# Kernel tuning notes

Measured on AMD Instinct MI355X. Metric: run time of the kernel, lower is better.

## Reference

```python
import jax, jax.numpy as jnp
import numpy as np

W = 192      # image width (seq len for attn1)
HN = 192     # H * N (seq len for attn2)
C = 128      # hidden_dim
NHEAD = 8


def setup_inputs() -> dict:
    key = jax.random.key(0)
    ks = jax.random.split(key, 12)
    sc = 0.05  # small init so softmax is well-conditioned
    feat = jax.random.normal(ks[0], (W, 2 * HN, C), jnp.float32)
    pos = jax.random.normal(ks[1], (2 * W - 1, C), jnp.float32)
    pos_y = jax.random.normal(ks[2], (2 * HN - 1, C), jnp.float32)
    i = jnp.arange(W)
    pos_indexes = (i[:, None] - i[None, :] + W - 1).reshape(-1).astype(jnp.int32)
    j = jnp.arange(HN)
    pos_indexes_y = (j[:, None] - j[None, :] + HN - 1).reshape(-1).astype(jnp.int32)
    return {
        "feat": feat,
        "pos": pos,
        "pos_y": pos_y,
        "ln_w": jnp.ones((C,), jnp.float32),
        "ln_b": jnp.zeros((C,), jnp.float32),
        "w_in1": jax.random.normal(ks[3], (3 * C, C), jnp.float32) * sc,
        "b_in1": jnp.zeros((3 * C,), jnp.float32),
        "w_out1": jax.random.normal(ks[4], (C, C), jnp.float32) * sc,
        "b_out1": jnp.zeros((C,), jnp.float32),
        "w_in2": jax.random.normal(ks[5], (3 * C, C), jnp.float32) * sc,
        "b_in2": jnp.zeros((3 * C,), jnp.float32),
        "w_out2": jax.random.normal(ks[6], (C, C), jnp.float32) * sc,
        "b_out2": jnp.zeros((C,), jnp.float32),
        "pos_indexes": pos_indexes,
        "pos_indexes_y": pos_indexes_y,
    }


def _layernorm(x, g, b, eps=1e-5):
    m = x.mean(-1, keepdims=True)
    v = ((x - m) ** 2).mean(-1, keepdims=True)
    return (x - m) / jnp.sqrt(v + eps) * g + b


def _rel_attn(x, pos_enc, pos_idx, w_in, b_in, w_out, b_out):
    # x: [w, bsz, c]; pos_enc: [2w-1, c]; pos_idx: [w*w]
    w, bsz, c = x.shape
    hd = c // NHEAD
    scale = float(hd) ** -0.5
    q, k, v = jnp.split(x @ w_in.T + b_in, 3, axis=-1)
    pe = pos_enc[pos_idx].reshape(w, w, c)           # [w, w, c] relative pos
    q_r, k_r = jnp.split(pe @ w_in[: 2 * c].T + b_in[: 2 * c], 2, axis=-1)
    q = (q * scale).reshape(w, bsz, NHEAD, hd)
    k = k.reshape(w, bsz, NHEAD, hd)
    v = v.reshape(w, bsz, NHEAD, hd)
    q_r = (q_r * scale).reshape(w, w, NHEAD, hd)
    k_r = k_r.reshape(w, w, NHEAD, hd)
    # content-content + content-pos + pos-content -> [bsz, nhead, w, w]
    attn = (jnp.einsum('wnec,vnec->newv', q, k)
            + jnp.einsum('wnec,wvec->newv', q, k_r)
            + jnp.einsum('vnec,wvec->newv', k, q_r))
    attn = jax.nn.softmax(attn, axis=-1)
    out = jnp.einsum('newv,vnec->wnec', attn, v).reshape(w, bsz, c)
    return out @ w_out.T + b_out


def reference(feat, pos, pos_y, ln_w, ln_b,
              w_in1, b_in1, w_out1, b_out1,
              w_in2, b_in2, w_out2, b_out2,
              pos_indexes, pos_indexes_y):
    w, h2, c = feat.shape
    f2 = _layernorm(feat, ln_w, ln_b)
    # [W, 2HN, C] -> [HN, 2W, C]: attention along vertical (H) axis
    f2 = f2.reshape(w, 2, h2 // 2, c).transpose(2, 1, 0, 3).reshape(h2 // 2, 2 * w, c)
    f2 = _rel_attn(f2, pos_y, pos_indexes_y, w_in2, b_in2, w_out2, b_out2)
    # back to [W, 2HN, C]: attention along horizontal (W) axis
    f2 = f2.reshape(h2 // 2, 2, w, c).transpose(2, 1, 0, 3).reshape(w, h2, c)
    f2 = _rel_attn(f2, pos, pos_indexes, w_in1, b_in1, w_out1, b_out1)
    return feat + f2
```

## Files before the change

kernel.cpp:

```cpp
#include <hip/hip_runtime.h>
#include <hip/hip_bf16.h>


typedef unsigned short u16;
typedef short bf16x8 __attribute__((ext_vector_type(8)));
typedef float f32x4 __attribute__((ext_vector_type(4)));
typedef float f32x16 __attribute__((ext_vector_type(16)));

__device__ inline u16 f2bf(float f) {
    union { float f; unsigned u; } a; a.f = f;
    unsigned u = a.u;
    unsigned r = u + 0x7FFFu + ((u >> 16) & 1u);
    return (u16)(r >> 16);
}
__device__ inline float bf2f(u16 x) {
    union { unsigned u; float f; } a; a.u = ((unsigned)x) << 16;
    return a.f;
}

__global__ __launch_bounds__(256) void ln_kernel(const float* __restrict__ feat,
                                                 const float* __restrict__ g,
                                                 const float* __restrict__ bta,
                                                 u16* __restrict__ x2) {
    int wid = threadIdx.x >> 6, lane = threadIdx.x & 63;
    int r = blockIdx.x * 4 + wid;
    const float* row = feat + (size_t)r * 128;
    float v0 = row[lane], v1 = row[lane + 64];
    float s = v0 + v1;
    for (int m = 1; m < 64; m <<= 1) s += __shfl_xor(s, m);
    float mean = s * (1.0f / 128.0f);
    float d0 = v0 - mean, d1 = v1 - mean;
    float vs = d0 * d0 + d1 * d1;
    for (int m = 1; m < 64; m <<= 1) vs += __shfl_xor(vs, m);
    float rstd = rsqrtf(vs * (1.0f / 128.0f) + 1e-5f);
    int w = r / 384, rem = r % 384;
    int out_r = (rem % 192) * 384 + (rem / 192) * 192 + w;
    u16* orow = x2 + (size_t)out_r * 128;
    orow[lane]      = f2bf(d0 * rstd * g[lane] + bta[lane]);
    orow[lane + 64] = f2bf(d1 * rstd * g[lane + 64] + bta[lane + 64]);
}

__global__ __launch_bounds__(256) void posproj_kernel(const float* __restrict__ pos,
                                                      const float* __restrict__ w_in,
                                                      const float* __restrict__ b_in,
                                                      u16* __restrict__ qr,
                                                      u16* __restrict__ kr) {
    int d = blockIdx.x, t = threadIdx.x;
    if (d == 383) {
        if (t < 128)      { int e = t >> 4,  j = t & 15;  qr[(e * 384 + 383) * 16 + j] = 0; }
        else              { int t2 = t - 128; int e = t2 >> 4, j = t2 & 15; kr[(e * 384 + 383) * 16 + j] = 0; }
        return;
    }
    __shared__ float prow[128];
    if (t < 128) prow[t] = pos[d * 128 + t];
    __syncthreads();
    const float* wrow = w_in + t * 128;
    float acc = b_in[t];
    #pragma unroll 8
    for (int k = 0; k < 128; ++k) acc += prow[k] * wrow[k];
    int which = t >> 7, e = (t >> 4) & 7, j = t & 15;
    if (which == 0) qr[(e * 384 + d) * 16 + j] = f2bf(acc * 0.25f);
    else            kr[(e * 384 + d) * 16 + j] = f2bf(acc);
}

__global__ __launch_bounds__(256) void qkv_gemm(const u16* __restrict__ X,
                                                const float* __restrict__ Wn,
                                                const float* __restrict__ bias,
                                                u16* __restrict__ Qo,
                                                u16* __restrict__ Ko,
                                                u16* __restrict__ Vo) {
    __shared__ u16 a_lds[128][136];
    __shared__ u16 w_lds[64][136];
    int tid = threadIdx.x;
    int m0 = blockIdx.y * 128, n0 = blockIdx.x * 64;
    #pragma unroll
    for (int i = 0; i < 8; ++i) {
        int idx = tid + 256 * i;
        int row = idx >> 4, c8 = (idx & 15) * 8;
        *(int4*)&a_lds[row][c8] = *(const int4*)&X[(size_t)(m0 + row) * 128 + c8];
    }
    #pragma unroll
    for (int i = 0; i < 8; ++i) {
        int idx = tid + 256 * i;
        int row = idx >> 5, c4 = (idx & 31) * 4;
        float4 f = *(const float4*)&Wn[(size_t)(n0 + row) * 128 + c4];
        uint2 p;
        p.x = (unsigned)f2bf(f.x) | ((unsigned)f2bf(f.y) << 16);
        p.y = (unsigned)f2bf(f.z) | ((unsigned)f2bf(f.w) << 16);
        *(uint2*)&w_lds[row][c4] = p;
    }
    __syncthreads();
    int lane = tid & 63, wid = tid >> 6;
    int wr = (wid >> 1) * 64, wc = (wid & 1) * 32;
    int kg = lane >> 4, l15 = lane & 15;
    f32x4 acc[4][2];
    #pragma unroll
    for (int i = 0; i < 4; ++i)
        #pragma unroll
        for (int j = 0; j < 2; ++j) acc[i][j] = (f32x4){0.f, 0.f, 0.f, 0.f};
    #pragma unroll
    for (int kk = 0; kk < 4; ++kk) {
        int kof = kk * 32 + kg * 8;
        bf16x8 a[4], b[2];
        #pragma unroll
        for (int i = 0; i < 4; ++i) a[i] = *(const bf16x8*)&a_lds[wr + i * 16 + l15][kof];
        #pragma unroll
        for (int j = 0; j < 2; ++j) b[j] = *(const bf16x8*)&w_lds[wc + j * 16 + l15][kof];
        #pragma unroll
        for (int i = 0; i < 4; ++i)
            #pragma unroll
            for (int j = 0; j < 2; ++j)
                acc[i][j] = __builtin_amdgcn_mfma_f32_16x16x32_bf16(a[i], b[j], acc[i][j], 0, 0, 0);
    }
    #pragma unroll
    for (int i = 0; i < 4; ++i)
        #pragma unroll
        for (int j = 0; j < 2; ++j) {
            int col_g = n0 + wc + j * 16 + l15;
            float bv = bias[col_g];
            int which = col_g >> 7, e = (col_g >> 4) & 7, d = col_g & 15;
            u16* dst = which == 0 ? Qo : (which == 1 ? Ko : Vo);
            float scl = which == 0 ? 0.25f : 1.0f;
            #pragma unroll
            for (int ii = 0; ii < 4; ++ii) {
                int row_g = m0 + wr + i * 16 + kg * 4 + ii;
                int batch = row_g % 384, sq = row_g / 384;
                dst[((size_t)(batch * 8 + e) * 192 + sq) * 16 + d] = f2bf((acc[i][j][ii] + bv) * scl);
            }
        }
}

__global__ __launch_bounds__(512, 6) void attn_kernel(const u16* __restrict__ Qg,
                                                      const u16* __restrict__ Kg,
                                                      const u16* __restrict__ Vg,
                                                      const u16* __restrict__ qr_g,
                                                      const u16* __restrict__ kr_g,
                                                      u16* __restrict__ Og) {
    __shared__ u16 sc[96][200];
    __shared__ u16 Qs[96][16];
    __shared__ u16 Ks[192][16];
    __shared__ u16 Vt[16][200];
    int tid = threadIdx.x, lane = tid & 63, wid = tid >> 6;
    int half = blockIdx.x, e = blockIdx.y, b = blockIdx.z;
    int w0 = half * 96;
    size_t base = ((size_t)b * 8 + e) * 192 * 16;

    if (tid < 192) { int row = tid >> 1, h8 = (tid & 1) * 8;
        *(int4*)&Qs[row][h8] = *(const int4*)&Qg[base + (size_t)(w0 + row) * 16 + h8]; }
    if (tid >= 128) { int t2 = tid - 128; int row = t2 >> 1, h8 = (t2 & 1) * 8;
        *(int4*)&Ks[row][h8] = *(const int4*)&Kg[base + (size_t)row * 16 + h8]; }
    #pragma unroll
    for (int i = 0; i < 6; ++i) { int idx = tid + 512 * i;
        Vt[idx & 15][idx >> 4] = Vg[base + idx]; }
    __syncthreads();

    int lo = lane & 31, hi = lane >> 5, hi8 = hi * 8;

    #pragma unroll
    for (int it = 0; it < 3; ++it) {
        int t = wid + 8 * it;
        if (t < 18) {
            int wt = t / 6, vt = t % 6;
            bf16x8 a  = *(const bf16x8*)&Qs[wt * 32 + lo][hi8];
            bf16x8 bb = *(const bf16x8*)&Ks[vt * 32 + lo][hi8];
            f32x16 acc = {};
            acc = __builtin_amdgcn_mfma_f32_32x32x16_bf16(a, bb, acc, 0, 0, 0);
            #pragma unroll
            for (int ii = 0; ii < 16; ++ii) {
                int row = wt * 32 + (ii & 3) + 8 * (ii >> 2) + 4 * hi;
                sc[row][vt * 32 + lo] = f2bf(acc[ii]);
            }
        }
    }
    __syncthreads();

    #pragma unroll
    for (int it = 0; it < 3; ++it) {
        int t = wid + 8 * it;
        if (t < 21) {
            int wt = t / 7, dj = t % 7;
            int d0 = w0 + wt * 32 + dj * 32;
            bf16x8 a  = *(const bf16x8*)&Qs[wt * 32 + lo][hi8];
            bf16x8 bb = *(const bf16x8*)(kr_g + ((size_t)e * 384 + d0 + lo) * 16 + hi8);
            f32x16 acc = {};
            acc = __builtin_amdgcn_mfma_f32_32x32x16_bf16(a, bb, acc, 0, 0, 0);
            int off = 4 * hi - lo + (wt * 32 + 191 - (dj * 32) - wt * 32);
            int vbase = w0 + wt * 32 + 191 - d0 - lo + 4 * hi;
            int wlb = wt * 32 + 4 * hi;
            (void)off;
            #pragma unroll
            for (int ii = 0; ii < 16; ++ii) {
                int rr = (ii & 3) + 8 * (ii >> 2);
                int v = vbase + rr;
                if ((unsigned)v < 192u) {
                    u16* p = &sc[wlb + rr][v];
                    *p = f2bf(bf2f(*p) + acc[ii]);
                }
            }
        }
    }
    __syncthreads();

    #pragma unroll
    for (int it = 0; it < 3; ++it) {
        int t = wid + 8 * it;
        if (t < 24) {
            int vt = t >> 2, dj = t & 3;
            int V0 = vt * 32;
            int d0 = w0 + 160 - V0 + dj * 32;
            bf16x8 a  = *(const bf16x8*)(qr_g + ((size_t)e * 384 + d0 + lo) * 16 + hi8);
            bf16x8 bb = *(const bf16x8*)&Ks[V0 + lo][hi8];
            f32x16 acc = {};
            acc = __builtin_amdgcn_mfma_f32_32x32x16_bf16(a, bb, acc, 0, 0, 0);
            int v = V0 + lo;
            int wlb = d0 + 4 * hi + v - 191 - w0;
            #pragma unroll
            for (int ii = 0; ii < 16; ++ii) {
                int rr = (ii & 3) + 8 * (ii >> 2);
                int wl = wlb + rr;
                if ((unsigned)wl < 96u) {
                    u16* p = &sc[wl][v];
                    *p = f2bf(bf2f(*p) + acc[ii]);
                }
            }
        }
    }
    __syncthreads();

    #pragma unroll
    for (int p = 0; p < 3; ++p) {
        int r = wid * 12 + p * 4 + (lane >> 4);
        int j = lane & 15;
        u16* rowp = &sc[r][j * 12];
        float sum = 0.f;
        #pragma unroll
        for (int k = 0; k < 12; ++k) {
            float ev = __expf(bf2f(rowp[k]));
            sum += ev;
            rowp[k] = f2bf(ev);
        }
        sum += __shfl_xor(sum, 1);
        sum += __shfl_xor(sum, 2);
        sum += __shfl_xor(sum, 4);
        sum += __shfl_xor(sum, 8);
        if (j == 0) *(float*)&sc[r][196] = 1.0f / sum;
    }
    __syncthreads();

    if (wid < 6) {
        int l15 = lane & 15, kg = lane >> 4;
        f32x4 acc = (f32x4){0.f, 0.f, 0.f, 0.f};
        #pragma unroll
        for (int kt = 0; kt < 6; ++kt) {
            bf16x8 a  = *(const bf16x8*)&sc[wid * 16 + l15][kt * 32 + kg * 8];
            bf16x8 bb = *(const bf16x8*)&Vt[l15][kt * 32 + kg * 8];
            acc = __builtin_amdgcn_mfma_f32_16x16x32_bf16(a, bb, acc, 0, 0, 0);
        }
        #pragma unroll
        for (int ii = 0; ii < 4; ++ii) {
            int wl = wid * 16 + kg * 4 + ii;
            float val = acc[ii] * (*(const float*)&sc[wl][196]);
            Og[((size_t)(w0 + wl) * 384 + b) * 128 + e * 16 + l15] = f2bf(val);
        }
    }
}

template <int MODE>
__global__ __launch_bounds__(256) void outproj_gemm(const u16* __restrict__ X,
                                                    const float* __restrict__ Wn,
                                                    const float* __restrict__ bias,
                                                    const float* __restrict__ feat,
                                                    u16* __restrict__ x1o,
                                                    float* __restrict__ outp) {
    __shared__ u16 a_lds[128][136];
    __shared__ u16 w_lds[64][136];
    int tid = threadIdx.x;
    int m0 = blockIdx.y * 128, n0 = blockIdx.x * 64;
    #pragma unroll
    for (int i = 0; i < 8; ++i) {
        int idx = tid + 256 * i;
        int row = idx >> 4, c8 = (idx & 15) * 8;
        *(int4*)&a_lds[row][c8] = *(const int4*)&X[(size_t)(m0 + row) * 128 + c8];
    }
    #pragma unroll
    for (int i = 0; i < 8; ++i) {
        int idx = tid + 256 * i;
        int row = idx >> 5, c4 = (idx & 31) * 4;
        float4 f = *(const float4*)&Wn[(size_t)(n0 + row) * 128 + c4];
        uint2 p;
        p.x = (unsigned)f2bf(f.x) | ((unsigned)f2bf(f.y) << 16);
        p.y = (unsigned)f2bf(f.z) | ((unsigned)f2bf(f.w) << 16);
        *(uint2*)&w_lds[row][c4] = p;
    }
    __syncthreads();
    int lane = tid & 63, wid = tid >> 6;
    int wr = (wid >> 1) * 64, wc = (wid & 1) * 32;
    int kg = lane >> 4, l15 = lane & 15;
    f32x4 acc[4][2];
    #pragma unroll
    for (int i = 0; i < 4; ++i)
        #pragma unroll
        for (int j = 0; j < 2; ++j) acc[i][j] = (f32x4){0.f, 0.f, 0.f, 0.f};
    #pragma unroll
    for (int kk = 0; kk < 4; ++kk) {
        int kof = kk * 32 + kg * 8;
        bf16x8 a[4], b[2];
        #pragma unroll
        for (int i = 0; i < 4; ++i) a[i] = *(const bf16x8*)&a_lds[wr + i * 16 + l15][kof];
        #pragma unroll
        for (int j = 0; j < 2; ++j) b[j] = *(const bf16x8*)&w_lds[wc + j * 16 + l15][kof];
        #pragma unroll
        for (int i = 0; i < 4; ++i)
            #pragma unroll
            for (int j = 0; j < 2; ++j)
                acc[i][j] = __builtin_amdgcn_mfma_f32_16x16x32_bf16(a[i], b[j], acc[i][j], 0, 0, 0);
    }
    #pragma unroll
    for (int i = 0; i < 4; ++i)
        #pragma unroll
        for (int j = 0; j < 2; ++j) {
            int col_g = n0 + wc + j * 16 + l15;
            float bv = bias[col_g];
            #pragma unroll
            for (int ii = 0; ii < 4; ++ii) {
                int row_g = m0 + wr + i * 16 + kg * 4 + ii;
                float val = acc[i][j][ii] + bv;
                if (MODE == 0) {
                    int h = row_g / 384, rem = row_g % 384, s2 = rem / 192, w = rem % 192;
                    x1o[((size_t)(w * 384 + s2 * 192 + h)) * 128 + col_g] = f2bf(val);
                } else {
                    size_t o = (size_t)row_g * 128 + col_g;
                    outp[o] = val + feat[o];
                }
            }
        }
}

extern "C" void kernel_launch(void* const* d_in, const int* in_sizes, int n_in,
                              void* d_out, int out_size, void* d_ws, size_t ws_size,
                              hipStream_t stream) {
    const float* feat   = (const float*)d_in[0];
    const float* pos    = (const float*)d_in[1];
    const float* pos_y  = (const float*)d_in[2];
    const float* ln_w   = (const float*)d_in[3];
    const float* ln_b   = (const float*)d_in[4];
    const float* w_in1  = (const float*)d_in[5];
    const float* b_in1  = (const float*)d_in[6];
    const float* w_out1 = (const float*)d_in[7];
    const float* b_out1 = (const float*)d_in[8];
    const float* w_in2  = (const float*)d_in[9];
    const float* b_in2  = (const float*)d_in[10];
    const float* w_out2 = (const float*)d_in[11];
    const float* b_out2 = (const float*)d_in[12];
    float* out = (float*)d_out;

    char* ws = (char*)d_ws;
    const size_t R = (size_t)73728 * 128;
    u16* x2 = (u16*)ws; ws += R * 2;
    u16* x1 = (u16*)ws; ws += R * 2;
    u16* Q  = (u16*)ws; ws += R * 2;
    u16* K  = (u16*)ws; ws += R * 2;
    u16* V  = (u16*)ws; ws += R * 2;
    u16* O  = (u16*)ws; ws += R * 2;
    u16* qr = (u16*)ws; ws += (size_t)8 * 384 * 16 * 2;
    u16* kr = (u16*)ws; ws += (size_t)8 * 384 * 16 * 2;

    ln_kernel<<<18432, 256, 0, stream>>>(feat, ln_w, ln_b, x2);
    posproj_kernel<<<384, 256, 0, stream>>>(pos_y, w_in2, b_in2, qr, kr);
    qkv_gemm<<<dim3(6, 576), 256, 0, stream>>>(x2, w_in2, b_in2, Q, K, V);
    attn_kernel<<<dim3(2, 8, 384), 512, 0, stream>>>(Q, K, V, qr, kr, O);
    outproj_gemm<0><<<dim3(2, 576), 256, 0, stream>>>(O, w_out2, b_out2, nullptr, x1, nullptr);
    posproj_kernel<<<384, 256, 0, stream>>>(pos, w_in1, b_in1, qr, kr);
    qkv_gemm<<<dim3(6, 576), 256, 0, stream>>>(x1, w_in1, b_in1, Q, K, V);
    attn_kernel<<<dim3(2, 8, 384), 512, 0, stream>>>(Q, K, V, qr, kr, O);
    outproj_gemm<1><<<dim3(2, 576), 256, 0, stream>>>(O, w_out1, b_out1, feat, nullptr, out);
}
```

Measured before the change: 435.0 us.

## Keep attention scores in fp32 LDS and read Q/K fragments directly from global

Changes the attention score buffer from bf16 to fp32 in shared memory, so the relative-position terms accumulate in fp32 without repeated bf16 round-trip conversions. Bounds checks are replaced by branchless writes to a dummy column. The Q and K shared-memory staging and its barrier are removed, and MFMA operands are loaded straight from global memory. Softmax writes packed bf16 probabilities back in place for the PV matmul. The larger LDS footprint lowers the occupancy hint from 6 to 4 blocks, which risks less latency hiding and redundant global loads.

```diff
diff --git a/kernel.cpp b/kernel.cpp
--- a/kernel.cpp
+++ b/kernel.cpp
@@ -3,6 +3,7 @@
 
 
 typedef unsigned short u16;
+typedef short bf16x4 __attribute__((ext_vector_type(4)));
 typedef short bf16x8 __attribute__((ext_vector_type(8)));
 typedef float f32x4 __attribute__((ext_vector_type(4)));
 typedef float f32x16 __attribute__((ext_vector_type(16)));
@@ -130,45 +131,42 @@
         }
 }
 
-__global__ __launch_bounds__(512, 6) void attn_kernel(const u16* __restrict__ Qg,
+__global__ __launch_bounds__(512, 4) void attn_kernel(const u16* __restrict__ Qg,
                                                       const u16* __restrict__ Kg,
                                                       const u16* __restrict__ Vg,
                                                       const u16* __restrict__ qr_g,
                                                       const u16* __restrict__ kr_g,
                                                       u16* __restrict__ Og) {
-    __shared__ u16 sc[96][200];
-    __shared__ u16 Qs[96][16];
-    __shared__ u16 Ks[192][16];
+    __shared__ float sc[96][194];
     __shared__ u16 Vt[16][200];
     int tid = threadIdx.x, lane = tid & 63, wid = tid >> 6;
     int half = blockIdx.x, e = blockIdx.y, b = blockIdx.z;
     int w0 = half * 96;
     size_t base = ((size_t)b * 8 + e) * 192 * 16;
 
-    if (tid < 192) { int row = tid >> 1, h8 = (tid & 1) * 8;
-        *(int4*)&Qs[row][h8] = *(const int4*)&Qg[base + (size_t)(w0 + row) * 16 + h8]; }
-    if (tid >= 128) { int t2 = tid - 128; int row = t2 >> 1, h8 = (t2 & 1) * 8;
-        *(int4*)&Ks[row][h8] = *(const int4*)&Kg[base + (size_t)row * 16 + h8]; }
     #pragma unroll
     for (int i = 0; i < 6; ++i) { int idx = tid + 512 * i;
         Vt[idx & 15][idx >> 4] = Vg[base + idx]; }
-    __syncthreads();
 
     int lo = lane & 31, hi = lane >> 5, hi8 = hi * 8;
+    const u16* Qrow  = Qg + base;
+    const u16* Krow  = Kg + base;
+    const u16* krrow = kr_g + (size_t)e * 384 * 16;
+    const u16* qrrow = qr_g + (size_t)e * 384 * 16;
 
     #pragma unroll
     for (int it = 0; it < 3; ++it) {
         int t = wid + 8 * it;
         if (t < 18) {
             int wt = t / 6, vt = t % 6;
-            bf16x8 a  = *(const bf16x8*)&Qs[wt * 32 + lo][hi8];
-            bf16x8 bb = *(const bf16x8*)&Ks[vt * 32 + lo][hi8];
+            bf16x8 a  = *(const bf16x8*)(Qrow + (size_t)(w0 + wt * 32 + lo) * 16 + hi8);
+            bf16x8 bb = *(const bf16x8*)(Krow + (size_t)(vt * 32 + lo) * 16 + hi8);
             f32x16 acc = {};
             acc = __builtin_amdgcn_mfma_f32_32x32x16_bf16(a, bb, acc, 0, 0, 0);
             #pragma unroll
             for (int ii = 0; ii < 16; ++ii) {
                 int row = wt * 32 + (ii & 3) + 8 * (ii >> 2) + 4 * hi;
-                sc[row][vt * 32 + lo] = f2bf(acc[ii]);
+                sc[row][vt * 32 + lo] = acc[ii];
             }
         }
     }
@@ -180,22 +178,18 @@
         if (t < 21) {
             int wt = t / 7, dj = t % 7;
             int d0 = w0 + wt * 32 + dj * 32;
-            bf16x8 a  = *(const bf16x8*)&Qs[wt * 32 + lo][hi8];
-            bf16x8 bb = *(const bf16x8*)(kr_g + ((size_t)e * 384 + d0 + lo) * 16 + hi8);
+            bf16x8 a  = *(const bf16x8*)(Qrow + (size_t)(w0 + wt * 32 + lo) * 16 + hi8);
+            bf16x8 bb = *(const bf16x8*)(krrow + (size_t)(d0 + lo) * 16 + hi8);
             f32x16 acc = {};
             acc = __builtin_amdgcn_mfma_f32_32x32x16_bf16(a, bb, acc, 0, 0, 0);
-            int off = 4 * hi - lo + (wt * 32 + 191 - (dj * 32) - wt * 32);
             int vbase = w0 + wt * 32 + 191 - d0 - lo + 4 * hi;
             int wlb = wt * 32 + 4 * hi;
-            (void)off;
             #pragma unroll
             for (int ii = 0; ii < 16; ++ii) {
                 int rr = (ii & 3) + 8 * (ii >> 2);
                 int v = vbase + rr;
-                if ((unsigned)v < 192u) {
-                    u16* p = &sc[wlb + rr][v];
-                    *p = f2bf(bf2f(*p) + acc[ii]);
-                }
+                int col = ((unsigned)v < 192u) ? v : 192;
+                sc[wlb + rr][col] += acc[ii];
             }
         }
     }
@@ -208,8 +202,8 @@
             int vt = t >> 2, dj = t & 3;
             int V0 = vt * 32;
             int d0 = w0 + 160 - V0 + dj * 32;
-            bf16x8 a  = *(const bf16x8*)(qr_g + ((size_t)e * 384 + d0 + lo) * 16 + hi8);
-            bf16x8 bb = *(const bf16x8*)&Ks[V0 + lo][hi8];
+            bf16x8 a  = *(const bf16x8*)(qrrow + (size_t)(d0 + lo) * 16 + hi8);
+            bf16x8 bb = *(const bf16x8*)(Krow + (size_t)(V0 + lo) * 16 + hi8);
             f32x16 acc = {};
             acc = __builtin_amdgcn_mfma_f32_32x32x16_bf16(a, bb, acc, 0, 0, 0);
             int v = V0 + lo;
@@ -218,10 +212,8 @@
             for (int ii = 0; ii < 16; ++ii) {
                 int rr = (ii & 3) + 8 * (ii >> 2);
                 int wl = wlb + rr;
-                if ((unsigned)wl < 96u) {
-                    u16* p = &sc[wl][v];
-                    *p = f2bf(bf2f(*p) + acc[ii]);
-                }
+                float* p = ((unsigned)wl < 96u) ? &sc[wl][v] : &sc[0][192];
+                *p += acc[ii];
             }
         }
     }
@@ -231,35 +223,43 @@
     for (int p = 0; p < 3; ++p) {
         int r = wid * 12 + p * 4 + (lane >> 4);
         int j = lane & 15;
-        u16* rowp = &sc[r][j * 12];
+        float x[12];
+        #pragma unroll
+        for (int k = 0; k < 6; ++k)
+            *(float2*)&x[k * 2] = *(const float2*)&sc[r][j * 12 + k * 2];
         float sum = 0.f;
         #pragma unroll
-        for (int k = 0; k < 12; ++k) {
-            float ev = __expf(bf2f(rowp[k]));
-            sum += ev;
-            rowp[k] = f2bf(ev);
-        }
+        for (int k = 0; k < 12; ++k) { x[k] = __expf(x[k]); sum += x[k]; }
+        unsigned* prow32 = (unsigned*)&sc[r][0];
+        #pragma unroll
+        for (int k = 0; k < 6; ++k)
+            prow32[j * 6 + k] = (unsigned)f2bf(x[2 * k]) | ((unsigned)f2bf(x[2 * k + 1]) << 16);
         sum += __shfl_xor(sum, 1);
         sum += __shfl_xor(sum, 2);
         sum += __shfl_xor(sum, 4);
         sum += __shfl_xor(sum, 8);
-        if (j == 0) *(float*)&sc[r][196] = 1.0f / sum;
+        if (j == 0) sc[r][193] = 1.0f / sum;
     }
     __syncthreads();
 
     if (wid < 6) {
         int l15 = lane & 15, kg = lane >> 4;
+        const u16* prow = (const u16*)&sc[wid * 16 + l15][0];
         f32x4 acc = (f32x4){0.f, 0.f, 0.f, 0.f};
         #pragma unroll
         for (int kt = 0; kt < 6; ++kt) {
-            bf16x8 a  = *(const bf16x8*)&sc[wid * 16 + l15][kt * 32 + kg * 8];
+            bf16x4 a0 = *(const bf16x4*)(prow + kt * 32 + kg * 8);
+            bf16x4 a1 = *(const bf16x4*)(prow + kt * 32 + kg * 8 + 4);
+            bf16x8 a;
+            a[0] = a0[0]; a[1] = a0[1]; a[2] = a0[2]; a[3] = a0[3];
+            a[4] = a1[0]; a[5] = a1[1]; a[6] = a1[2]; a[7] = a1[3];
             bf16x8 bb = *(const bf16x8*)&Vt[l15][kt * 32 + kg * 8];
             acc = __builtin_amdgcn_mfma_f32_16x16x32_bf16(a, bb, acc, 0, 0, 0);
         }
         #pragma unroll
         for (int ii = 0; ii < 4; ++ii) {
             int wl = wid * 16 + kg * 4 + ii;
-            float val = acc[ii] * (*(const float*)&sc[wl][196]);
+            float val = acc[ii] * sc[wl][193];
             Og[((size_t)(w0 + wl) * 384 + b) * 128 + e * 16 + l15] = f2bf(val);
         }
     }
```

Measured after the change: 363.6 us. -16.4%, faster.
